# Performance work log

Measured on AMD Instinct MI355X. Metric: run time of the kernel, lower is better.

The kernel has to match this reference:

```python
import jax, jax.numpy as jnp
import numpy as np
from jax import lax

B, IMG, ED, NC = 32, 224, 256, 10
DI, DS, DC, DR = 512, 64, 4, 16   # d_inner, d_state, d_conv, dt_rank
NB, L = 6, (IMG // 16) ** 2       # 6 mamba blocks, seq len 196
EPS = 1e-5


def setup_inputs():
    key = jax.random.key(0)
    ks = iter(jax.random.split(key, 48))
    def rn(shape, s=0.02):
        return jax.random.normal(next(ks), shape, jnp.float32) * s
    def ru(shape):
        return jax.random.uniform(next(ks), shape, jnp.float32, 0.5, 1.5)
    inp = {"x": jax.random.normal(next(ks), (B, 3, IMG, IMG), jnp.float32)}
    c = [ED // 4, ED // 2, ED]
    for i, (ci, co) in enumerate([(3, c[0]), (c[0], c[1]), (c[1], c[2])], 1):
        inp[f"c{i}w"] = rn((co, ci, 3, 3), 0.05)
        inp[f"c{i}b"] = rn((co,))
        inp[f"b{i}g"] = jnp.ones((co,), jnp.float32)
        inp[f"b{i}b"] = jnp.zeros((co,), jnp.float32)
        inp[f"b{i}m"] = rn((co,))
        inp[f"b{i}v"] = ru((co,))
    inp["ln_g"] = jnp.ones((NB, ED), jnp.float32)
    inp["ln_b"] = jnp.zeros((NB, ED), jnp.float32)
    inp["w_in"] = rn((NB, 2 * DI, ED))
    inp["cw"] = rn((NB, DI, DC), 0.1)
    inp["cb"] = rn((NB, DI))
    inp["w_x"] = rn((NB, DR + 2 * DS, DI))
    inp["w_dt"] = rn((NB, DI, DR), 0.1)
    inp["b_dt"] = rn((NB, DI), 0.5)
    inp["a_log"] = jnp.tile(jnp.log(jnp.arange(1, DS + 1, dtype=jnp.float32)), (NB, DI, 1))
    inp["d_skip"] = jnp.ones((NB, DI), jnp.float32)
    inp["w_out"] = rn((NB, ED, DI))
    inp["fc_w"] = rn((NC, ED))
    inp["fc_b"] = jnp.zeros((NC,), jnp.float32)
    return inp


def _conv2d(x, w, s, p):
    return lax.conv_general_dilated(x, w, (s, s), [(p, p), (p, p)],
                                    dimension_numbers=("NCHW", "OIHW", "NCHW"))


def _bn(x, g, b, m, v):
    sh = (1, -1, 1, 1)
    return (x - m.reshape(sh)) * (g.reshape(sh) / jnp.sqrt(v.reshape(sh) + EPS)) + b.reshape(sh)


def _maxpool(x, k, s, p):
    return lax.reduce_window(x, -jnp.inf, lax.max, (1, 1, k, k), (1, 1, s, s),
                             [(0, 0), (0, 0), (p, p), (p, p)])


def _mamba_block(x, ln_g, ln_b, w_in, cw, cb, w_x, w_dt, b_dt, a_log, d_skip, w_out):
    res = x
    mu = x.mean(-1, keepdims=True)
    var = ((x - mu) ** 2).mean(-1, keepdims=True)
    h = (x - mu) / jnp.sqrt(var + EPS) * ln_g + ln_b
    xz = jnp.einsum("bld,ed->ble", h, w_in)            # [B,L,2*DI]
    xi, z = xz[..., :DI], xz[..., DI:]
    # causal depthwise conv1d (pad left DC-1) + silu
    xt = lax.conv_general_dilated(xi.transpose(0, 2, 1), cw[:, None, :], (1,),
                                  [(DC - 1, 0)], dimension_numbers=("NCH", "OIH", "NCH"),
                                  feature_group_count=DI) + cb[None, :, None]
    xc = jax.nn.silu(xt).transpose(0, 2, 1)            # [B,L,DI]
    dbl = jnp.einsum("bld,ed->ble", xc, w_x)           # [B,L,DR+2*DS]
    dt = jax.nn.softplus(jnp.einsum("blr,dr->bld", dbl[..., :DR], w_dt) + b_dt)
    Bm = dbl[..., DR:DR + DS]                          # [B,L,DS]
    Cm = dbl[..., DR + DS:]                            # [B,L,DS]
    A = -jnp.exp(a_log)                                # [DI,DS]

    def step(hst, ins):
        dt_t, b_t, c_t, x_t = ins                      # [B,DI],[B,DS],[B,DS],[B,DI]
        dA = jnp.exp(dt_t[..., None] * A)              # [B,DI,DS]
        hst = dA * hst + (dt_t * x_t)[..., None] * b_t[:, None, :]
        return hst, jnp.einsum("bds,bs->bd", hst, c_t)

    h0 = jnp.zeros((x.shape[0], DI, DS), x.dtype)
    _, ys = lax.scan(step, h0, (dt.transpose(1, 0, 2), Bm.transpose(1, 0, 2),
                                Cm.transpose(1, 0, 2), xc.transpose(1, 0, 2)))
    y = ys.transpose(1, 0, 2) + d_skip * xc
    y = y * jax.nn.silu(z)
    return jnp.einsum("bld,ed->ble", y, w_out) + res


def reference(x, c1w, c1b, b1g, b1b, b1m, b1v, c2w, c2b, b2g, b2b, b2m, b2v,
              c3w, c3b, b3g, b3b, b3m, b3v, ln_g, ln_b, w_in, cw, cb, w_x,
              w_dt, b_dt, a_log, d_skip, w_out, fc_w, fc_b):
    h = _maxpool(jax.nn.relu(_bn(_conv2d(x, c1w, 2, 1) + c1b.reshape(1, -1, 1, 1), b1g, b1b, b1m, b1v)), 3, 2, 1)
    h = _maxpool(jax.nn.relu(_bn(_conv2d(h, c2w, 1, 1) + c2b.reshape(1, -1, 1, 1), b2g, b2b, b2m, b2v)), 2, 2, 0)
    h = _maxpool(jax.nn.relu(_bn(_conv2d(h, c3w, 1, 1) + c3b.reshape(1, -1, 1, 1), b3g, b3b, b3m, b3v)), 2, 2, 0)
    h = h.reshape(h.shape[0], ED, -1).transpose(0, 2, 1)   # [B,L,ED]
    for i in range(NB):
        h = _mamba_block(h, ln_g[i], ln_b[i], w_in[i], cw[i], cb[i], w_x[i],
                         w_dt[i], b_dt[i], a_log[i], d_skip[i], w_out[i])
    h = h.mean(axis=1)                                     # adaptive avg pool over L
    return h @ fc_w.T + fc_b
```

## Files before the change

kernel.cpp:

```cpp
#include <hip/hip_runtime.h>

typedef __bf16 bf16x8 __attribute__((ext_vector_type(8)));
typedef float f32x4 __attribute__((ext_vector_type(4)));

#define EPS 1e-5f

__device__ __forceinline__ unsigned short f2bu(float f) {
  union { float f; unsigned u; } x; x.f = f;
  unsigned r = x.u + 0x7fffu + ((x.u >> 16) & 1u);
  return (unsigned short)(r >> 16);
}
__device__ __forceinline__ float bu2f(unsigned short u) {
  union { unsigned u; float f; } x; x.u = ((unsigned)u) << 16;
  return x.f;
}

__device__ __forceinline__ void gld16(const void* g, void* l) {
  __builtin_amdgcn_global_load_lds((const __attribute__((address_space(1))) void*)g,
                                   (__attribute__((address_space(3))) void*)l, 16, 0, 0);
}

__global__ __launch_bounds__(256) void k_prep(
    const float* __restrict__ w_in, unsigned short* __restrict__ w_in_bf,
    const float* __restrict__ w_x, unsigned short* __restrict__ w_x_bf,
    const float* __restrict__ w_out, unsigned short* __restrict__ w_out_bf,
    const float* __restrict__ c2w, unsigned short* __restrict__ w2p,
    const float* __restrict__ c3w, unsigned short* __restrict__ w3p,
    const float* __restrict__ w_dt, float* __restrict__ wdt_t) {
  int id = blockIdx.x * 256 + threadIdx.x;
  if (id < 1572864) { w_in_bf[id] = f2bu(w_in[id]); return; }
  id -= 1572864;
  if (id < 442368) { w_x_bf[id] = f2bu(w_x[id]); return; }
  id -= 442368;
  if (id < 786432) { w_out_bf[id] = f2bu(w_out[id]); return; }
  id -= 786432;
  if (id < 73728) {
    int ci = id % 64, tap = (id / 64) % 9, co = id / 576;
    w2p[id] = f2bu(c2w[(co * 64 + ci) * 9 + tap]);
    return;
  }
  id -= 73728;
  if (id < 294912) {
    int ci = id % 128, tap = (id / 128) % 9, co = id / 1152;
    w3p[id] = f2bu(c3w[(co * 128 + ci) * 9 + tap]);
    return;
  }
  id -= 294912;
  {
    int d = id & 511, r = (id >> 9) & 15, blk = id >> 13;
    wdt_t[id] = w_dt[(blk * 512 + d) * 16 + r];
  }
}

__global__ __launch_bounds__(256) void k_conv1a(
    const float* __restrict__ x, const float* __restrict__ w,
    const float* __restrict__ cb, const float* __restrict__ g,
    const float* __restrict__ bb, const float* __restrict__ bm_,
    const float* __restrict__ bv, unsigned short* __restrict__ out) {
  __shared__ __align__(16) float sx[9][228];
  __shared__ float sw[64 * 27];
  __shared__ float sa[64], sb[64];
  int tid = threadIdx.x;
  int oy = blockIdx.x % 112, b = blockIdx.x / 112;
  for (int i = tid; i < 9 * 228; i += 256) {
    int row = i / 228;
    int ixl = i - row * 228;
    int ci = row / 3, ky = row - ci * 3;
    int iy = 2 * oy - 1 + ky;
    int ix = ixl - 1;
    float v = 0.f;
    if ((unsigned)iy < 224u && (unsigned)ix < 224u)
      v = x[((size_t)(b * 3 + ci) * 224 + iy) * 224 + ix];
    sx[row][ixl] = v;
  }
  for (int i = tid; i < 64 * 27; i += 256) sw[i] = w[i];
  if (tid < 64) {
    int c = tid;
    float alpha = g[c] * rsqrtf(bv[c] + EPS);
    sa[c] = alpha;
    sb[c] = (cb[c] - bm_[c]) * alpha + bb[c];
  }
  __syncthreads();
  int c = tid & 63, grp = tid >> 6;
  int ox0 = grp * 28;
  float acc[28];
#pragma unroll
  for (int i = 0; i < 28; ++i) acc[i] = 0.f;
#pragma unroll
  for (int ci = 0; ci < 3; ++ci) {
    float wr[9];
#pragma unroll
    for (int j = 0; j < 9; ++j) wr[j] = sw[c * 27 + ci * 9 + j];
#pragma unroll
    for (int ky = 0; ky < 3; ++ky) {
      const float* row = sx[ci * 3 + ky];
#pragma unroll
      for (int q = 0; q < 7; ++q) {
        int base = 2 * (ox0 + q * 4);
        f32x4 a0 = *(const f32x4*)&row[base];
        f32x4 a1 = *(const f32x4*)&row[base + 4];
        f32x4 a2 = *(const f32x4*)&row[base + 8];
        float xv[12] = {a0[0], a0[1], a0[2], a0[3], a1[0], a1[1],
                        a1[2], a1[3], a2[0], a2[1], a2[2], a2[3]};
#pragma unroll
        for (int p = 0; p < 4; ++p) {
          acc[q * 4 + p] = fmaf(xv[2 * p + 0], wr[ky * 3 + 0], acc[q * 4 + p]);
          acc[q * 4 + p] = fmaf(xv[2 * p + 1], wr[ky * 3 + 1], acc[q * 4 + p]);
          acc[q * 4 + p] = fmaf(xv[2 * p + 2], wr[ky * 3 + 2], acc[q * 4 + p]);
        }
      }
    }
  }
  float alpha = sa[c], beta = sb[c];
  unsigned short* op = out + (((size_t)(b * 112 + oy)) * 112 + ox0) * 64 + c;
#pragma unroll
  for (int p = 0; p < 28; ++p)
    op[(size_t)p * 64] = f2bu(fmaxf(acc[p] * alpha + beta, 0.f));
}

__global__ __launch_bounds__(256) void k_pool3(const unsigned short* __restrict__ in,
                                               unsigned short* __restrict__ out) {
  int id = blockIdx.x * 256 + threadIdx.x;
  int c = id & 63;
  int t = id >> 6;
  int px = t % 56; t /= 56;
  int py = t % 56;
  int b = t / 56;
  float m = 0.f;
#pragma unroll
  for (int ky = 0; ky < 3; ++ky) {
    int iy = py * 2 - 1 + ky;
    if ((unsigned)iy >= 112u) continue;
#pragma unroll
    for (int kx = 0; kx < 3; ++kx) {
      int ix = px * 2 - 1 + kx;
      if ((unsigned)ix >= 112u) continue;
      m = fmaxf(m, bu2f(in[(((size_t)(b * 112 + iy) * 112) + ix) * 64 + c]));
    }
  }
  out[id] = f2bu(m);
}

template <int H, int Wd, int CI, int CO>
__global__ __launch_bounds__(256) void k_convgemm(
    const unsigned short* __restrict__ In, const unsigned short* __restrict__ Wt,
    const float* __restrict__ cb, const float* __restrict__ g,
    const float* __restrict__ bb, const float* __restrict__ bm_,
    const float* __restrict__ bv, unsigned short* __restrict__ Out) {
  constexpr int K = 9 * CI;
  constexpr int NTN = CO / 64;
  int bm = blockIdx.x / NTN, bn = blockIdx.x - bm * NTN;
  int lane = threadIdx.x & 63, wid = threadIdx.x >> 6;
  int wr = wid >> 1, wc = wid & 1;
  int r0 = bm * 64 + wr * 32 + (lane & 15);
  int r1 = r0 + 16;
  int c0 = bn * 64 + wc * 32 + (lane & 15);
  int koff = (lane >> 4) << 3;
  int ox0 = r0 % Wd; int t0 = r0 / Wd; int oy0 = t0 % H; int b0 = t0 / H;
  int ox1 = r1 % Wd; int t1 = r1 / Wd; int oy1 = t1 % H; int b1 = t1 / H;
  const unsigned short* pb0 = Wt + (size_t)c0 * K + koff;
  const unsigned short* pb1 = Wt + (size_t)(c0 + 16) * K + koff;
  f32x4 acc[2][2] = {};
  for (int k0 = 0; k0 < K; k0 += 32) {
    int k = k0 + koff;
    int tap = k / CI;
    int ci = k - tap * CI;
    int ky = tap / 3, kx = tap - ky * 3;
    int iy0 = oy0 + ky - 1, ix0 = ox0 + kx - 1;
    int iy1 = oy1 + ky - 1, ix1 = ox1 + kx - 1;
    bf16x8 a0 = {};
    bf16x8 a1 = {};
    if ((unsigned)iy0 < (unsigned)H && (unsigned)ix0 < (unsigned)Wd)
      a0 = *(const bf16x8*)(In + ((size_t)((b0 * H + iy0) * Wd + ix0)) * CI + ci);
    if ((unsigned)iy1 < (unsigned)H && (unsigned)ix1 < (unsigned)Wd)
      a1 = *(const bf16x8*)(In + ((size_t)((b1 * H + iy1) * Wd + ix1)) * CI + ci);
    bf16x8 w0 = *(const bf16x8*)(pb0 + k0);
    bf16x8 w1 = *(const bf16x8*)(pb1 + k0);
    acc[0][0] = __builtin_amdgcn_mfma_f32_16x16x32_bf16(a0, w0, acc[0][0], 0, 0, 0);
    acc[0][1] = __builtin_amdgcn_mfma_f32_16x16x32_bf16(a0, w1, acc[0][1], 0, 0, 0);
    acc[1][0] = __builtin_amdgcn_mfma_f32_16x16x32_bf16(a1, w0, acc[1][0], 0, 0, 0);
    acc[1][1] = __builtin_amdgcn_mfma_f32_16x16x32_bf16(a1, w1, acc[1][1], 0, 0, 0);
  }
  int rr = (lane >> 4) * 4, rc = lane & 15;
#pragma unroll
  for (int tj = 0; tj < 2; ++tj) {
    int col = bn * 64 + wc * 32 + tj * 16 + rc;
    float alpha = g[col] * rsqrtf(bv[col] + EPS);
    float beta = (cb[col] - bm_[col]) * alpha + bb[col];
#pragma unroll
    for (int ti = 0; ti < 2; ++ti) {
      int row = bm * 64 + wr * 32 + ti * 16 + rr;
#pragma unroll
      for (int r = 0; r < 4; ++r) {
        float v = fmaxf(acc[ti][tj][r] * alpha + beta, 0.f);
        Out[(size_t)(row + r) * CO + col] = f2bu(v);
      }
    }
  }
}

template <int H, int Wd, int C, bool OUTF>
__global__ __launch_bounds__(256) void k_pool(const unsigned short* __restrict__ in,
                                              void* __restrict__ outv) {
  constexpr int OH = H / 2, OW = Wd / 2;
  int id = blockIdx.x * 256 + threadIdx.x;
  int c = id % C;
  int t = id / C;
  int px = t % OW; t /= OW;
  int py = t % OH;
  int b = t / OH;
  const unsigned short* p = in + (((size_t)(b * H + py * 2) * Wd) + px * 2) * C + c;
  float m0 = bu2f(p[0]), m1 = bu2f(p[C]);
  float m2 = bu2f(p[(size_t)Wd * C]), m3 = bu2f(p[(size_t)Wd * C + C]);
  float m = fmaxf(fmaxf(m0, m1), fmaxf(m2, m3));
  if (OUTF) ((float*)outv)[id] = m;
  else ((unsigned short*)outv)[id] = f2bu(m);
}

__global__ __launch_bounds__(256) void k_ln(const float* __restrict__ h,
                                            const float* __restrict__ g,
                                            const float* __restrict__ b2,
                                            unsigned short* __restrict__ out) {
  int lane = threadIdx.x & 63, wid = threadIdx.x >> 6;
  int t = blockIdx.x * 4 + wid;
  float4 v = *(const float4*)(h + (size_t)t * 256 + lane * 4);
  float s = v.x + v.y + v.z + v.w;
  float q = v.x * v.x + v.y * v.y + v.z * v.z + v.w * v.w;
#pragma unroll
  for (int off = 32; off; off >>= 1) {
    s += __shfl_xor(s, off);
    q += __shfl_xor(q, off);
  }
  float mu = s * (1.f / 256.f);
  float var = q * (1.f / 256.f) - mu * mu;
  float rs = rsqrtf(var + EPS);
  float4 gg = *(const float4*)(g + lane * 4);
  float4 bb = *(const float4*)(b2 + lane * 4);
  ushort4 o;
  o.x = f2bu((v.x - mu) * rs * gg.x + bb.x);
  o.y = f2bu((v.y - mu) * rs * gg.y + bb.y);
  o.z = f2bu((v.z - mu) * rs * gg.z + bb.z);
  o.w = f2bu((v.w - mu) * rs * gg.w + bb.w);
  *(ushort4*)(out + (size_t)t * 256 + lane * 4) = o;
}

template <int BM, int BN, int KSTEPS, bool ADD>
__global__ __launch_bounds__(256) void k_sgemm(const unsigned short* __restrict__ A,
                                               const unsigned short* __restrict__ W,
                                               float* __restrict__ C,
                                               int N, int ntn) {
  constexpr int K = KSTEPS * 64;
  constexpr int MR = BM / 32;
  constexpr int NR = BN / 32;
  __shared__ __align__(16) unsigned short As[BM * 64];
  __shared__ __align__(16) unsigned short Bs[BN * 64];
  int bm = blockIdx.x / ntn, bn = blockIdx.x - bm * ntn;
  int lane = threadIdx.x & 63, wid = threadIdx.x >> 6;
  int wr = wid >> 1, wc = wid & 1;
  const int arow = lane >> 3, acol = (lane & 7) * 8;
  f32x4 acc[MR][NR] = {};
  const unsigned short* Abase = A + (size_t)(bm * BM) * K;
  const unsigned short* Wbase = W + (size_t)(bn * BN) * K;
  for (int t = 0; t < KSTEPS; ++t) {
    int k0 = t * 64;
#pragma unroll
    for (int i = 0; i < BM / 32; ++i) {
      int chunk = wid * (BM / 32) + i;
      gld16(Abase + (size_t)(chunk * 8 + arow) * K + k0 + acol, &As[chunk * 512 + lane * 8]);
    }
#pragma unroll
    for (int i = 0; i < BN / 32; ++i) {
      int chunk = wid * (BN / 32) + i;
      gld16(Wbase + (size_t)(chunk * 8 + arow) * K + k0 + acol, &Bs[chunk * 512 + lane * 8]);
    }
    __syncthreads();
#pragma unroll
    for (int kk = 0; kk < 2; ++kk) {
      bf16x8 af[MR], bfr[NR];
#pragma unroll
      for (int mi = 0; mi < MR; ++mi)
        af[mi] = *(const bf16x8*)&As[(wr * (BM / 2) + mi * 16 + (lane & 15)) * 64 + kk * 32 + (lane >> 4) * 8];
#pragma unroll
      for (int nj = 0; nj < NR; ++nj)
        bfr[nj] = *(const bf16x8*)&Bs[(wc * (BN / 2) + nj * 16 + (lane & 15)) * 64 + kk * 32 + (lane >> 4) * 8];
#pragma unroll
      for (int mi = 0; mi < MR; ++mi)
#pragma unroll
        for (int nj = 0; nj < NR; ++nj)
          acc[mi][nj] = __builtin_amdgcn_mfma_f32_16x16x32_bf16(af[mi], bfr[nj], acc[mi][nj], 0, 0, 0);
    }
    __syncthreads();
  }
  int rr = (lane >> 4) * 4, rc = lane & 15;
#pragma unroll
  for (int mi = 0; mi < MR; ++mi)
#pragma unroll
    for (int nj = 0; nj < NR; ++nj) {
      int row = bm * BM + wr * (BM / 2) + mi * 16 + rr;
      int col = bn * BN + wc * (BN / 2) + nj * 16 + rc;
#pragma unroll
      for (int r = 0; r < 4; ++r) {
        float v = acc[mi][nj][r];
        if (ADD) v += C[(size_t)(row + r) * N + col];
        C[(size_t)(row + r) * N + col] = v;
      }
    }
}

template <bool ADD_RES>
__global__ __launch_bounds__(256) void k_gemm(const unsigned short* __restrict__ A,
                                              const unsigned short* __restrict__ W,
                                              float* __restrict__ C, int M, int N,
                                              int K, int ntn) {
  int bm = blockIdx.x / ntn, bn = blockIdx.x - bm * ntn;
  int lane = threadIdx.x & 63, wid = threadIdx.x >> 6;
  int wr = wid >> 1, wc = wid & 1;
  int r0 = bm * 64 + wr * 32 + (lane & 15);
  int c0 = bn * 64 + wc * 32 + (lane & 15);
  int koff = (lane >> 4) << 3;
  int cc0 = (c0 < N) ? c0 : (N - 1);
  int cc1 = (c0 + 16 < N) ? (c0 + 16) : (N - 1);
  const unsigned short* pa0 = A + (size_t)r0 * K + koff;
  const unsigned short* pa1 = A + (size_t)(r0 + 16) * K + koff;
  const unsigned short* pb0 = W + (size_t)cc0 * K + koff;
  const unsigned short* pb1 = W + (size_t)cc1 * K + koff;
  f32x4 acc[2][2] = {};
  for (int k0 = 0; k0 < K; k0 += 32) {
    bf16x8 a0 = *(const bf16x8*)(pa0 + k0);
    bf16x8 a1 = *(const bf16x8*)(pa1 + k0);
    bf16x8 b0 = *(const bf16x8*)(pb0 + k0);
    bf16x8 b1 = *(const bf16x8*)(pb1 + k0);
    acc[0][0] = __builtin_amdgcn_mfma_f32_16x16x32_bf16(a0, b0, acc[0][0], 0, 0, 0);
    acc[0][1] = __builtin_amdgcn_mfma_f32_16x16x32_bf16(a0, b1, acc[0][1], 0, 0, 0);
    acc[1][0] = __builtin_amdgcn_mfma_f32_16x16x32_bf16(a1, b0, acc[1][0], 0, 0, 0);
    acc[1][1] = __builtin_amdgcn_mfma_f32_16x16x32_bf16(a1, b1, acc[1][1], 0, 0, 0);
  }
  int rr = (lane >> 4) * 4, rc = lane & 15;
#pragma unroll
  for (int ti = 0; ti < 2; ++ti)
#pragma unroll
    for (int tj = 0; tj < 2; ++tj) {
      int col = bn * 64 + wc * 32 + tj * 16 + rc;
      if (col >= N) continue;
      int row = bm * 64 + wr * 32 + ti * 16 + rr;
#pragma unroll
      for (int r = 0; r < 4; ++r) {
        float v = acc[ti][tj][r];
        if (ADD_RES) v += C[(size_t)(row + r) * N + col];
        C[(size_t)(row + r) * N + col] = v;
      }
    }
}

__global__ __launch_bounds__(256) void k_dwconv(const float* __restrict__ xz,
                                                const float* __restrict__ cw,
                                                const float* __restrict__ cb,
                                                float* __restrict__ xc,
                                                unsigned short* __restrict__ xcb) {
  int id = blockIdx.x * 256 + threadIdx.x;
  int d = id & 511;
  int bl = id >> 9;
  int l = bl % 196;
  int b = bl / 196;
  const float* xi = xz + (size_t)(b * 196) * 1024 + d;
  float4 c4 = *(const float4*)(cw + d * 4);
  float acc = cb[d];
  if (l >= 3) acc = fmaf(xi[(size_t)(l - 3) * 1024], c4.x, acc);
  if (l >= 2) acc = fmaf(xi[(size_t)(l - 2) * 1024], c4.y, acc);
  if (l >= 1) acc = fmaf(xi[(size_t)(l - 1) * 1024], c4.z, acc);
  acc = fmaf(xi[(size_t)l * 1024], c4.w, acc);
  float s = acc / (1.f + __expf(-acc));
  xc[id] = s;
  xcb[id] = f2bu(s);
}

__global__ __launch_bounds__(256) void k_dt(const float* __restrict__ dbl,
                                            const float* __restrict__ wt,
                                            const float* __restrict__ bdt,
                                            float* __restrict__ dt) {
  int id = blockIdx.x * 256 + threadIdx.x;
  int d = id & 511;
  int bl = id >> 9;
  const float4* a = (const float4*)(dbl + (size_t)bl * 144);
  float acc = bdt[d];
#pragma unroll
  for (int i = 0; i < 4; ++i) {
    float4 av = a[i];
    acc = fmaf(av.x, wt[(i * 4 + 0) * 512 + d], acc);
    acc = fmaf(av.y, wt[(i * 4 + 1) * 512 + d], acc);
    acc = fmaf(av.z, wt[(i * 4 + 2) * 512 + d], acc);
    acc = fmaf(av.w, wt[(i * 4 + 3) * 512 + d], acc);
  }
  dt[id] = fmaxf(acc, 0.f) + log1pf(__expf(-fabsf(acc)));
}

__global__ __launch_bounds__(1024) void k_scan(
    const float* __restrict__ dtb, const float* __restrict__ xc,
    const float* __restrict__ dbl, const float* __restrict__ xz,
    const float* __restrict__ a_log, const float* __restrict__ d_skip,
    unsigned short* __restrict__ y) {
  __shared__ float lds[16][584];
  int lane = threadIdx.x & 63, wid = threadIdx.x >> 6;
  int bid = blockIdx.x;
  int nbid = (bid & 7) * 128 + (bid >> 3);
  int wgid = nbid * 16 + wid;
  int b = wgid >> 9, d = wgid & 511;
  float A = -__expf(a_log[d * 64 + lane]);
  float dsk = d_skip[d];
  const float* dt_p = dtb + (size_t)(b * 196) * 512 + d;
  const float* xc_p = xc + (size_t)(b * 196) * 512 + d;
  const float* z_p = xz + (size_t)(b * 196) * 1024 + 512 + d;
  const float* bc_p = dbl + (size_t)(b * 196) * 144 + 16 + lane;
  unsigned short* y_p = y + (size_t)(b * 196) * 512 + d;
  float* L = lds[wid];
  float h = 0.f;
  int g = lane >> 3, j = lane & 7;
  const float* dt_c = dt_p;
  const float* xc_c = xc_p;
  const float* bc_c = bc_p;
  for (int t = 0; t < 24; ++t) {
    int l0 = t * 8;
    float p[8];
#pragma unroll
    for (int li = 0; li < 8; ++li) {
      float dtv = dt_c[li * 512];
      float xv = xc_c[li * 512];
      float Bv = bc_c[li * 144];
      float Cv = bc_c[li * 144 + 64];
      float dA = __expf(dtv * A);
      h = fmaf(dA, h, (dtv * xv) * Bv);
      p[li] = h * Cv;
    }
#pragma unroll
    for (int li = 0; li < 8; ++li) L[lane * 9 + li] = p[li];
    __builtin_amdgcn_wave_barrier();
    float s = 0.f;
#pragma unroll
    for (int k = 0; k < 8; ++k) s += L[(j * 8 + k) * 9 + g];
    __builtin_amdgcn_wave_barrier();
    s += __shfl_xor(s, 1);
    s += __shfl_xor(s, 2);
    s += __shfl_xor(s, 4);
    if (j == 0) {
      int l = l0 + g;
      float xv = xc_p[(size_t)l * 512];
      float zv = z_p[(size_t)l * 1024];
      float sig = 1.f / (1.f + __expf(-zv));
      y_p[(size_t)l * 512] = f2bu((s + dsk * xv) * (zv * sig));
    }
    dt_c += 8 * 512;
    xc_c += 8 * 512;
    bc_c += 8 * 144;
  }
  {
    float p[8];
#pragma unroll
    for (int li = 0; li < 8; ++li) {
      bool ok = (li < 4);
      float dtv = ok ? dt_c[li * 512] : 0.f;
      float xv = ok ? xc_c[li * 512] : 0.f;
      float Bv = ok ? bc_c[li * 144] : 0.f;
      float Cv = ok ? bc_c[li * 144 + 64] : 0.f;
      float dA = __expf(dtv * A);
      h = fmaf(dA, h, (dtv * xv) * Bv);
      p[li] = h * Cv;
    }
#pragma unroll
    for (int li = 0; li < 8; ++li) L[lane * 9 + li] = p[li];
    __builtin_amdgcn_wave_barrier();
    float s = 0.f;
#pragma unroll
    for (int k = 0; k < 8; ++k) s += L[(j * 8 + k) * 9 + g];
    __builtin_amdgcn_wave_barrier();
    s += __shfl_xor(s, 1);
    s += __shfl_xor(s, 2);
    s += __shfl_xor(s, 4);
    int l = 192 + g;
    if (j == 0 && l < 196) {
      float xv = xc_p[(size_t)l * 512];
      float zv = z_p[(size_t)l * 1024];
      float sig = 1.f / (1.f + __expf(-zv));
      y_p[(size_t)l * 512] = f2bu((s + dsk * xv) * (zv * sig));
    }
  }
}

__global__ __launch_bounds__(256) void k_mean2(const float* __restrict__ h,
                                               float* __restrict__ part) {
  int b = blockIdx.x >> 2, q = blockIdx.x & 3;
  int e = threadIdx.x;
  const float* hb = h + ((size_t)b * 196 + q * 49) * 256 + e;
  float s = 0.f;
  for (int l = 0; l < 49; ++l) s += hb[(size_t)l * 256];
  part[((size_t)b * 4 + q) * 256 + e] = s;
}

__global__ __launch_bounds__(256) void k_head(const float* __restrict__ part,
                                              const float* __restrict__ fw,
                                              const float* __restrict__ fb,
                                              float* __restrict__ out) {
  __shared__ float sp[256];
  int b = blockIdx.x;
  int tid = threadIdx.x, lane = tid & 63, w = tid >> 6;
  const float* pb = part + (size_t)b * 4 * 256;
  sp[tid] = (pb[tid] + pb[256 + tid] + pb[512 + tid] + pb[768 + tid]) * (1.f / 196.f);
  __syncthreads();
  for (int n = w; n < 10; n += 4) {
    float s = 0.f;
#pragma unroll
    for (int i = 0; i < 4; ++i) {
      int e = lane * 4 + i;
      e = e & 255;
      s += sp[e] * fw[n * 256 + e];
    }
    s += __shfl_xor(s, 1); s += __shfl_xor(s, 2); s += __shfl_xor(s, 4);
    s += __shfl_xor(s, 8); s += __shfl_xor(s, 16); s += __shfl_xor(s, 32);
    if (lane == 0) out[b * 10 + n] = s + fb[n];
  }
}

static inline unsigned cdiv(unsigned a, unsigned b) { return (a + b - 1) / b; }

extern "C" void kernel_launch(void* const* d_in, const int* in_sizes, int n_in,
                              void* d_out, int out_size, void* d_ws, size_t ws_size,
                              hipStream_t stream) {
  const float* x = (const float*)d_in[0];
  const float* c1w = (const float*)d_in[1]; const float* c1b = (const float*)d_in[2];
  const float* b1g = (const float*)d_in[3]; const float* b1b = (const float*)d_in[4];
  const float* b1m = (const float*)d_in[5]; const float* b1v = (const float*)d_in[6];
  const float* c2w = (const float*)d_in[7]; const float* c2b = (const float*)d_in[8];
  const float* b2g = (const float*)d_in[9]; const float* b2b = (const float*)d_in[10];
  const float* b2m = (const float*)d_in[11]; const float* b2v = (const float*)d_in[12];
  const float* c3w = (const float*)d_in[13]; const float* c3b = (const float*)d_in[14];
  const float* b3g = (const float*)d_in[15]; const float* b3b = (const float*)d_in[16];
  const float* b3m = (const float*)d_in[17]; const float* b3v = (const float*)d_in[18];
  const float* ln_g = (const float*)d_in[19]; const float* ln_b = (const float*)d_in[20];
  const float* w_in = (const float*)d_in[21];
  const float* cw = (const float*)d_in[22]; const float* cbv = (const float*)d_in[23];
  const float* w_x = (const float*)d_in[24];
  const float* w_dt = (const float*)d_in[25]; const float* b_dt = (const float*)d_in[26];
  const float* a_log = (const float*)d_in[27]; const float* d_skip = (const float*)d_in[28];
  const float* w_out = (const float*)d_in[29];
  const float* fc_w = (const float*)d_in[30]; const float* fc_b = (const float*)d_in[31];

  char* ws = (char*)d_ws;
  size_t off = 0;
  auto take = [&](size_t bytes) { size_t o = off; off += bytes; return o; };
  size_t S = take(67837952);
  unsigned short* c1o = (unsigned short*)(ws + S + 0);
  unsigned short* t1 = (unsigned short*)(ws + S + 51380224);
  unsigned short* t2 = (unsigned short*)(ws + S + 0);
  unsigned short* t3 = (unsigned short*)(ws + S + 25690112);
  unsigned short* t4 = (unsigned short*)(ws + S + 32112640);
  float* xz = (float*)(ws + S + 0);
  float* xc = (float*)(ws + S + 25690112);
  unsigned short* xcb = (unsigned short*)(ws + S + 38535168);
  float* dbl = (float*)(ws + S + 44957696);
  float* dtb = (float*)(ws + S + 48570368);
  unsigned short* ybf = (unsigned short*)(ws + S + 61415424);
  float* h = (float*)(ws + take(6422528));
  unsigned short* hbf = (unsigned short*)(ws + take(3211264));
  unsigned short* w_in_bf = (unsigned short*)(ws + take(3145728));
  unsigned short* w_x_bf = (unsigned short*)(ws + take(884736));
  unsigned short* w_out_bf = (unsigned short*)(ws + take(1572864));
  unsigned short* w2p = (unsigned short*)(ws + take(147456));
  unsigned short* w3p = (unsigned short*)(ws + take(589824));
  float* wdt_t = (float*)(ws + take(196608));
  float* part = (float*)(ws + take(131072));
  (void)ws_size; (void)in_sizes; (void)n_in; (void)out_size;

  k_prep<<<12576, 256, 0, stream>>>(w_in, w_in_bf, w_x, w_x_bf, w_out, w_out_bf,
                                    c2w, w2p, c3w, w3p, w_dt, wdt_t);

  k_conv1a<<<3584, 256, 0, stream>>>(x, c1w, c1b, b1g, b1b, b1m, b1v, c1o);
  k_pool3<<<25088, 256, 0, stream>>>(c1o, t1);
  k_convgemm<56, 56, 64, 128><<<1568 * 2, 256, 0, stream>>>(t1, w2p, c2b, b2g, b2b, b2m, b2v, t2);
  k_pool<56, 56, 128, false><<<12544, 256, 0, stream>>>(t2, t3);
  k_convgemm<28, 28, 128, 256><<<392 * 4, 256, 0, stream>>>(t3, w3p, c3b, b3g, b3b, b3m, b3v, t4);
  k_pool<28, 28, 256, true><<<6272, 256, 0, stream>>>(t4, h);

  for (int blk = 0; blk < 6; ++blk) {
    k_ln<<<1568, 256, 0, stream>>>(h, ln_g + blk * 256, ln_b + blk * 256, hbf);
    k_sgemm<128, 128, 4, false><<<49 * 8, 256, 0, stream>>>(
        hbf, w_in_bf + (size_t)blk * 1024 * 256, xz, 1024, 8);
    k_dwconv<<<12544, 256, 0, stream>>>(xz, cw + blk * 512 * 4, cbv + blk * 512, xc, xcb);
    k_gemm<false><<<98 * 3, 256, 0, stream>>>(xcb, w_x_bf + (size_t)blk * 144 * 512, dbl,
                                              6272, 144, 512, 3);
    k_dt<<<12544, 256, 0, stream>>>(dbl, wdt_t + blk * 8192, b_dt + blk * 512, dtb);
    k_scan<<<1024, 1024, 0, stream>>>(dtb, xc, dbl, xz, a_log + blk * 512 * 64,
                                      d_skip + blk * 512, ybf);
    k_sgemm<64, 64, 8, true><<<98 * 4, 256, 0, stream>>>(
        ybf, w_out_bf + (size_t)blk * 256 * 512, h, 256, 4);
  }

  k_mean2<<<128, 256, 0, stream>>>(h, part);
  k_head<<<32, 256, 0, stream>>>(part, fc_w, fc_b, (float*)d_out);
}
```

Baseline: 1.625 ms.

## Store dt and conv outputs channel-major so scan loads contiguous vectors

The depthwise conv and dt-projection kernels now use LDS tiles and write their fp32 outputs transposed to [B, D, L]. This lets each scan wave load its dt and xc sequence with contiguous 16-byte vector loads instead of strided scalar loads 2 KB apart. The producer kernels take on an LDS staging step and transposed writes, and each now launches only 1024 blocks, which may cut their parallelism.

```diff
diff --git a/kernel.cpp b/kernel.cpp
--- a/kernel.cpp
+++ b/kernel.cpp
@@ -352,50 +352,81 @@
     }
 }
 
-__global__ __launch_bounds__(256) void k_dwconv(const float* __restrict__ xz,
-                                                const float* __restrict__ cw,
-                                                const float* __restrict__ cb,
-                                                float* __restrict__ xc,
-                                                unsigned short* __restrict__ xcb) {
-  int id = blockIdx.x * 256 + threadIdx.x;
-  int d = id & 511;
-  int bl = id >> 9;
-  int l = bl % 196;
-  int b = bl / 196;
-  const float* xi = xz + (size_t)(b * 196) * 1024 + d;
-  float4 c4 = *(const float4*)(cw + d * 4);
-  float acc = cb[d];
-  if (l >= 3) acc = fmaf(xi[(size_t)(l - 3) * 1024], c4.x, acc);
-  if (l >= 2) acc = fmaf(xi[(size_t)(l - 2) * 1024], c4.y, acc);
-  if (l >= 1) acc = fmaf(xi[(size_t)(l - 1) * 1024], c4.z, acc);
-  acc = fmaf(xi[(size_t)l * 1024], c4.w, acc);
-  float s = acc / (1.f + __expf(-acc));
-  xc[id] = s;
-  xcb[id] = f2bu(s);
-}
-
-__global__ __launch_bounds__(256) void k_dt(const float* __restrict__ dbl,
-                                            const float* __restrict__ wt,
-                                            const float* __restrict__ bdt,
-                                            float* __restrict__ dt) {
-  int id = blockIdx.x * 256 + threadIdx.x;
-  int d = id & 511;
-  int bl = id >> 9;
-  const float4* a = (const float4*)(dbl + (size_t)bl * 144);
-  float acc = bdt[d];
-#pragma unroll
-  for (int i = 0; i < 4; ++i) {
-    float4 av = a[i];
-    acc = fmaf(av.x, wt[(i * 4 + 0) * 512 + d], acc);
-    acc = fmaf(av.y, wt[(i * 4 + 1) * 512 + d], acc);
-    acc = fmaf(av.z, wt[(i * 4 + 2) * 512 + d], acc);
-    acc = fmaf(av.w, wt[(i * 4 + 3) * 512 + d], acc);
-  }
-  dt[id] = fmaxf(acc, 0.f) + log1pf(__expf(-fabsf(acc)));
+__global__ __launch_bounds__(256) void k_dwconvT(const float* __restrict__ xz,
+                                                 const float* __restrict__ cw,
+                                                 const float* __restrict__ cb,
+                                                 float* __restrict__ xcT,
+                                                 unsigned short* __restrict__ xcb) {
+  __shared__ float sxz[52][67];
+  __shared__ float sxc[49][67];
+  int tid = threadIdx.x;
+  int l0 = blockIdx.x * 49, d0 = blockIdx.y * 64, b = blockIdx.z;
+  for (int i = tid; i < 52 * 64; i += 256) {
+    int row = i >> 6, dd = i & 63;
+    int gl = l0 - 3 + row;
+    float v = 0.f;
+    if (gl >= 0) v = xz[((size_t)(b * 196 + gl)) * 1024 + d0 + dd];
+    sxz[row][dd] = v;
+  }
+  __syncthreads();
+  int lane = tid & 63, wv = tid >> 6;
+#pragma unroll
+  for (int i = 0; i < 16; ++i) {
+    int dl = wv * 16 + i;
+    int d = d0 + dl;
+    float4 c4 = *(const float4*)(cw + d * 4);
+    float acc = cb[d];
+    acc = fmaf(sxz[lane + 0][dl], c4.x, acc);
+    acc = fmaf(sxz[lane + 1][dl], c4.y, acc);
+    acc = fmaf(sxz[lane + 2][dl], c4.z, acc);
+    acc = fmaf(sxz[lane + 3][dl], c4.w, acc);
+    float s = acc / (1.f + __expf(-acc));
+    if (lane < 49) {
+      xcT[((size_t)(b * 512 + d)) * 196 + l0 + lane] = s;
+      sxc[lane][dl] = s;
+    }
+  }
+  __syncthreads();
+  for (int i = tid; i < 49 * 64; i += 256) {
+    int row = i >> 6, dd = i & 63;
+    xcb[((size_t)(b * 196 + l0 + row)) * 512 + d0 + dd] = f2bu(sxc[row][dd]);
+  }
+}
+
+__global__ __launch_bounds__(256) void k_dtT(const float* __restrict__ dbl,
+                                             const float* __restrict__ wt,
+                                             const float* __restrict__ bdt,
+                                             float* __restrict__ dtT) {
+  __shared__ float sdbl[49][17];
+  __shared__ float swdt[16][64];
+  __shared__ float sbdt[64];
+  int tid = threadIdx.x;
+  int l0 = blockIdx.x * 49, d0 = blockIdx.y * 64, b = blockIdx.z;
+  for (int i = tid; i < 49 * 16; i += 256) {
+    int row = i >> 4, r = i & 15;
+    sdbl[row][r] = dbl[((size_t)(b * 196 + l0 + row)) * 144 + r];
+  }
+  for (int i = tid; i < 16 * 64; i += 256) {
+    int r = i >> 6, dd = i & 63;
+    swdt[r][dd] = wt[r * 512 + d0 + dd];
+  }
+  if (tid < 64) sbdt[tid] = bdt[d0 + tid];
+  __syncthreads();
+  int lane = tid & 63, wv = tid >> 6;
+#pragma unroll
+  for (int i = 0; i < 16; ++i) {
+    int dl = wv * 16 + i;
+    float acc = sbdt[dl];
+#pragma unroll
+    for (int r = 0; r < 16; ++r) acc = fmaf(sdbl[lane < 49 ? lane : 0][r], swdt[r][dl], acc);
+    float sp = fmaxf(acc, 0.f) + log1pf(__expf(-fabsf(acc)));
+    if (lane < 49)
+      dtT[((size_t)(b * 512 + d0 + dl)) * 196 + l0 + lane] = sp;
+  }
 }
 
 __global__ __launch_bounds__(1024) void k_scan(
-    const float* __restrict__ dtb, const float* __restrict__ xc,
+    const float* __restrict__ dtT, const float* __restrict__ xcT,
     const float* __restrict__ dbl, const float* __restrict__ xz,
     const float* __restrict__ a_log, const float* __restrict__ d_skip,
     unsigned short* __restrict__ y) {
@@ -407,28 +438,30 @@
   int b = wgid >> 9, d = wgid & 511;
   float A = -__expf(a_log[d * 64 + lane]);
   float dsk = d_skip[d];
-  const float* dt_p = dtb + (size_t)(b * 196) * 512 + d;
-  const float* xc_p = xc + (size_t)(b * 196) * 512 + d;
+  const float* dtr = dtT + (size_t)(b * 512 + d) * 196;
+  const float* xcr = xcT + (size_t)(b * 512 + d) * 196;
   const float* z_p = xz + (size_t)(b * 196) * 1024 + 512 + d;
   const float* bc_p = dbl + (size_t)(b * 196) * 144 + 16 + lane;
   unsigned short* y_p = y + (size_t)(b * 196) * 512 + d;
   float* L = lds[wid];
   float h = 0.f;
   int g = lane >> 3, j = lane & 7;
-  const float* dt_c = dt_p;
-  const float* xc_c = xc_p;
   const float* bc_c = bc_p;
   for (int t = 0; t < 24; ++t) {
     int l0 = t * 8;
+    f32x4 dq0 = *(const f32x4*)(dtr + l0);
+    f32x4 dq1 = *(const f32x4*)(dtr + l0 + 4);
+    f32x4 xq0 = *(const f32x4*)(xcr + l0);
+    f32x4 xq1 = *(const f32x4*)(xcr + l0 + 4);
+    float dtv[8] = {dq0[0], dq0[1], dq0[2], dq0[3], dq1[0], dq1[1], dq1[2], dq1[3]};
+    float xvv[8] = {xq0[0], xq0[1], xq0[2], xq0[3], xq1[0], xq1[1], xq1[2], xq1[3]};
     float p[8];
 #pragma unroll
     for (int li = 0; li < 8; ++li) {
-      float dtv = dt_c[li * 512];
-      float xv = xc_c[li * 512];
       float Bv = bc_c[li * 144];
       float Cv = bc_c[li * 144 + 64];
-      float dA = __expf(dtv * A);
-      h = fmaf(dA, h, (dtv * xv) * Bv);
+      float dA = __expf(dtv[li] * A);
+      h = fmaf(dA, h, (dtv[li] * xvv[li]) * Bv);
       p[li] = h * Cv;
     }
 #pragma unroll
@@ -443,26 +476,26 @@
     s += __shfl_xor(s, 4);
     if (j == 0) {
       int l = l0 + g;
-      float xv = xc_p[(size_t)l * 512];
+      float xv = xcr[l];
       float zv = z_p[(size_t)l * 1024];
       float sig = 1.f / (1.f + __expf(-zv));
       y_p[(size_t)l * 512] = f2bu((s + dsk * xv) * (zv * sig));
     }
-    dt_c += 8 * 512;
-    xc_c += 8 * 512;
     bc_c += 8 * 144;
   }
   {
+    f32x4 dq0 = *(const f32x4*)(dtr + 192);
+    f32x4 xq0 = *(const f32x4*)(xcr + 192);
+    float dtv[8] = {dq0[0], dq0[1], dq0[2], dq0[3], 0.f, 0.f, 0.f, 0.f};
+    float xvv[8] = {xq0[0], xq0[1], xq0[2], xq0[3], 0.f, 0.f, 0.f, 0.f};
     float p[8];
 #pragma unroll
     for (int li = 0; li < 8; ++li) {
       bool ok = (li < 4);
-      float dtv = ok ? dt_c[li * 512] : 0.f;
-      float xv = ok ? xc_c[li * 512] : 0.f;
       float Bv = ok ? bc_c[li * 144] : 0.f;
       float Cv = ok ? bc_c[li * 144 + 64] : 0.f;
-      float dA = __expf(dtv * A);
-      h = fmaf(dA, h, (dtv * xv) * Bv);
+      float dA = __expf(dtv[li] * A);
+      h = fmaf(dA, h, (dtv[li] * xvv[li]) * Bv);
       p[li] = h * Cv;
     }
 #pragma unroll
@@ -477,7 +510,7 @@
     s += __shfl_xor(s, 4);
     int l = 192 + g;
     if (j == 0 && l < 196) {
-      float xv = xc_p[(size_t)l * 512];
+      float xv = xcr[l];
       float zv = z_p[(size_t)l * 1024];
       float sig = 1.f / (1.f + __expf(-zv));
       y_p[(size_t)l * 512] = f2bu((s + dsk * xv) * (zv * sig));
@@ -553,10 +586,10 @@
   unsigned short* t3 = (unsigned short*)(ws + S + 25690112);
   unsigned short* t4 = (unsigned short*)(ws + S + 32112640);
   float* xz = (float*)(ws + S + 0);
-  float* xc = (float*)(ws + S + 25690112);
+  float* xcT = (float*)(ws + S + 25690112);
   unsigned short* xcb = (unsigned short*)(ws + S + 38535168);
   float* dbl = (float*)(ws + S + 44957696);
-  float* dtb = (float*)(ws + S + 48570368);
+  float* dtT = (float*)(ws + S + 48570368);
   unsigned short* ybf = (unsigned short*)(ws + S + 61415424);
   float* h = (float*)(ws + take(6422528));
   unsigned short* hbf = (unsigned short*)(ws + take(3211264));
@@ -583,11 +616,12 @@
     k_ln<<<1568, 256, 0, stream>>>(h, ln_g + blk * 256, ln_b + blk * 256, hbf);
     k_sgemm<128, 128, 4, false><<<49 * 8, 256, 0, stream>>>(
         hbf, w_in_bf + (size_t)blk * 1024 * 256, xz, 1024, 8);
-    k_dwconv<<<12544, 256, 0, stream>>>(xz, cw + blk * 512 * 4, cbv + blk * 512, xc, xcb);
+    k_dwconvT<<<dim3(4, 8, 32), 256, 0, stream>>>(xz, cw + blk * 512 * 4, cbv + blk * 512,
+                                                  xcT, xcb);
     k_gemm<false><<<98 * 3, 256, 0, stream>>>(xcb, w_x_bf + (size_t)blk * 144 * 512, dbl,
                                               6272, 144, 512, 3);
-    k_dt<<<12544, 256, 0, stream>>>(dbl, wdt_t + blk * 8192, b_dt + blk * 512, dtb);
-    k_scan<<<1024, 1024, 0, stream>>>(dtb, xc, dbl, xz, a_log + blk * 512 * 64,
+    k_dtT<<<dim3(4, 8, 32), 256, 0, stream>>>(dbl, wdt_t + blk * 8192, b_dt + blk * 512, dtT);
+    k_scan<<<1024, 1024, 0, stream>>>(dtT, xcT, dbl, xz, a_log + blk * 512 * 64,
                                       d_skip + blk * 512, ybf);
     k_sgemm<64, 64, 8, true><<<98 * 4, 256, 0, stream>>>(
         ybf, w_out_bf + (size_t)blk * 256 * 512, h, 256, 4);
```

Result: faster. 1.575 ms (-3.1%).
